# Kernel optimization log

Measured on AMD Instinct MI355X. Metric: run time of the kernel, lower is better.

## Reference

```python
import jax, jax.numpy as jnp
import numpy as np

VOCAB = 67
EMB = 32
BRANCH = 32
OUT = 96
L = 16
B = 131072


def setup_inputs() -> dict:
    key = jax.random.key(0)
    ks = jax.random.split(key, 10)
    x = jax.random.randint(ks[0], (B, L), 0, VOCAB, dtype=jnp.int64)
    embed = jax.random.normal(ks[1], (VOCAB, EMB), dtype=jnp.float32) * 0.1
    w2 = jax.random.normal(ks[2], (BRANCH, EMB, 2), dtype=jnp.float32) * 0.1
    b2 = jnp.zeros((BRANCH,), jnp.float32)
    w3 = jax.random.normal(ks[3], (BRANCH, EMB, 3), dtype=jnp.float32) * 0.1
    b3 = jnp.zeros((BRANCH,), jnp.float32)
    w4 = jax.random.normal(ks[4], (BRANCH, EMB, 4), dtype=jnp.float32) * 0.1
    b4 = jnp.zeros((BRANCH,), jnp.float32)
    pw = jax.random.normal(ks[5], (OUT, 3 * BRANCH), dtype=jnp.float32) * 0.02
    pb = jnp.zeros((OUT,), jnp.float32)
    return {"x": x, "embed": embed, "w2": w2, "b2": b2, "w3": w3,
            "b3": b3, "w4": w4, "b4": b4, "pw": pw, "pb": pb}


def _branch(emb_ncl, w, b):
    # emb_ncl: [B, EMB, L]; w: [BRANCH, EMB, k] -> conv valid, ReLU, max over time
    y = jax.lax.conv_general_dilated(
        emb_ncl, w, window_strides=(1,), padding='VALID',
        dimension_numbers=('NCH', 'OIH', 'NCH'))
    y = jax.nn.relu(y + b[None, :, None])
    return jnp.max(y, axis=2)  # [B, BRANCH]


def reference(x, embed, w2, b2, w3, b3, w4, b4, pw, pb):
    # padding_idx=0: row 0 of the table is zeros
    table = embed.at[0].set(0.0)
    emb = table[x]                      # [B, L, EMB]
    emb = jnp.transpose(emb, (0, 2, 1))  # [B, EMB, L]
    g2 = _branch(emb, w2, b2)
    g3 = _branch(emb, w3, b3)
    g4 = _branch(emb, w4, b4)
    feat = jnp.concatenate([g2, g3, g4], axis=1)  # [B, 96]
    # Linear + ReLU (dropout is identity at eval)
    return jax.nn.relu(feat @ pw.T + pb)
```

## Files before the change

### kernel.cpp

```cpp
#include <hip/hip_runtime.h>
#include <hip/hip_fp16.h>


#define VOCABSZ 67
#define EMBSZ   32
#define NCH     32
#define NFEAT   96
#define SEQL    16
#define BATCH   131072
#define NTAB    9
#define NENT    (NTAB * VOCABSZ)
#define TABU    (NENT * NCH / 2)
#define PWOFF   TABU
#define NFP     (NFEAT / 2)
#define NPW     (NFEAT * NFP)
#define ESTR    80
#define LTS     (VOCABSZ * ESTR)
#define LDSB    (NTAB * LTS)

typedef _Float16 v2h __attribute__((ext_vector_type(2)));
typedef _Float16 v8h __attribute__((ext_vector_type(8)));
typedef float    v4f __attribute__((ext_vector_type(4)));

__device__ __forceinline__ unsigned packh2(float a, float b) {
    v2h p; p[0] = (_Float16)a; p[1] = (_Float16)b;
    return __builtin_bit_cast(unsigned, p);
}

__global__ __launch_bounds__(256) void build_tables(
    const float* __restrict__ embed,
    const float* __restrict__ w2, const float* __restrict__ b2,
    const float* __restrict__ w3, const float* __restrict__ b3,
    const float* __restrict__ w4, const float* __restrict__ b4,
    const float* __restrict__ pw,
    unsigned* __restrict__ ws)
{
    int idx = blockIdx.x * 256 + threadIdx.x;
    if (idx < TABU) {
        int cp = idx & 15;
        int t  = idx >> 4;
        int j  = t / VOCABSZ;
        int v  = t - j * VOCABSZ;
        const float* w; const float* bias; int k, h;
        if (j < 2)      { w = w2; k = 2; h = j;     bias = (h == 0) ? b2 : nullptr; }
        else if (j < 5) { w = w3; k = 3; h = j - 2; bias = (h == 0) ? b3 : nullptr; }
        else            { w = w4; k = 4; h = j - 5; bias = (h == 0) ? b4 : nullptr; }
        int c0 = 2 * cp;
        float a0 = bias ? bias[c0]     : 0.0f;
        float a1 = bias ? bias[c0 + 1] : 0.0f;
        if (v != 0) {
            #pragma unroll
            for (int e = 0; e < EMBSZ; ++e) {
                float ev = embed[v * EMBSZ + e];
                a0 += ev * w[((c0    ) * EMBSZ + e) * k + h];
                a1 += ev * w[((c0 + 1) * EMBSZ + e) * k + h];
            }
        }
        ws[t * 16 + cp] = packh2(a0, a1);
    } else if (idx < TABU + NPW) {
        int i  = idx - TABU;
        int o  = i / NFP;
        int fp = i - o * NFP;
        ws[PWOFF + i] = packh2(pw[o * NFEAT + 2 * fp], pw[o * NFEAT + 2 * fp + 1]);
    }
}

template<int K, int N, int P0, int TB>
__device__ __forceinline__ void lconv(const char* __restrict__ base,
                                      const int (&ap)[16], v8h& m)
{
    v8h s[N];
    #pragma unroll
    for (int u = 0; u < N; ++u)
        s[u] = *reinterpret_cast<const v8h*>(base + TB + ap[P0 + u]);
    #pragma unroll
    for (int h = 1; h < K; ++h) {
        v8h t[N];
        #pragma unroll
        for (int u = 0; u < N; ++u)
            t[u] = *reinterpret_cast<const v8h*>(base + TB + h * LTS + ap[P0 + u + h]);
        #pragma unroll
        for (int u = 0; u < N; ++u) s[u] = s[u] + t[u];
    }
    #pragma unroll
    for (int u = 0; u < N; ++u) m = __builtin_elementwise_max(m, s[u]);
}

__global__ __launch_bounds__(512, 6) void fused_cnn(
    const int*      __restrict__ x,
    const unsigned* __restrict__ ws,
    const float*    __restrict__ pb,
    float*          __restrict__ out)
{
    extern __shared__ __align__(16) char ldsraw[];
    const int tid = threadIdx.x;
    {
        const float4* s4 = reinterpret_cast<const float4*>(ws);
        float4* d4 = reinterpret_cast<float4*>(ldsraw);
        #pragma unroll
        for (int i0 = 0; i0 < 2560; i0 += 512) {
            int i = i0 + tid;
            if (i < 2412) {
                int t = i >> 2, c = i & 3;
                d4[5 * t + c] = s4[i];
            }
        }
    }
    __syncthreads();

    const int lane = tid & 63;
    const int wv   = tid >> 6;
    const int ml   = lane & 15;
    const int c    = lane >> 4;
    const int co   = c << 4;
    const int rowb = blockIdx.x * 128 + wv * 16;
    const int row  = rowb + ml;
    const char* base = ldsraw;

    const int4* xp = reinterpret_cast<const int4*>(x + row * SEQL);
    int4 q0 = xp[0], q1 = xp[1], q2 = xp[2], q3 = xp[3];
    int ap[16];
    ap[ 0] = q0.x * ESTR + co; ap[ 1] = q0.y * ESTR + co;
    ap[ 2] = q0.z * ESTR + co; ap[ 3] = q0.w * ESTR + co;
    ap[ 4] = q1.x * ESTR + co; ap[ 5] = q1.y * ESTR + co;
    ap[ 6] = q1.z * ESTR + co; ap[ 7] = q1.w * ESTR + co;
    ap[ 8] = q2.x * ESTR + co; ap[ 9] = q2.y * ESTR + co;
    ap[10] = q2.z * ESTR + co; ap[11] = q2.w * ESTR + co;
    ap[12] = q3.x * ESTR + co; ap[13] = q3.y * ESTR + co;
    ap[14] = q3.z * ESTR + co; ap[15] = q3.w * ESTR + co;

    v8h m2 = {}, m3 = {}, m4 = {};

    lconv<2, 5,  0, 0 * LTS>(base, ap, m2);
    lconv<2, 5,  5, 0 * LTS>(base, ap, m2);
    lconv<2, 5, 10, 0 * LTS>(base, ap, m2);
    lconv<3, 5,  0, 2 * LTS>(base, ap, m3);
    lconv<3, 5,  5, 2 * LTS>(base, ap, m3);
    lconv<3, 4, 10, 2 * LTS>(base, ap, m3);
    lconv<4, 5,  0, 5 * LTS>(base, ap, m4);
    lconv<4, 4,  5, 5 * LTS>(base, ap, m4);
    lconv<4, 4,  9, 5 * LTS>(base, ap, m4);

    const unsigned* __restrict__ pwp = ws + PWOFF + ml * NFP + c * 4;
    #pragma unroll
    for (int u = 0; u < 6; ++u) {
        v4f acc = {0.f, 0.f, 0.f, 0.f};
        v8h b0 = *reinterpret_cast<const v8h*>(pwp + 768 * u);
        v8h b1 = *reinterpret_cast<const v8h*>(pwp + 768 * u + 16);
        v8h b2 = *reinterpret_cast<const v8h*>(pwp + 768 * u + 32);
        acc = __builtin_amdgcn_mfma_f32_16x16x32_f16(m2, b0, acc, 0, 0, 0);
        acc = __builtin_amdgcn_mfma_f32_16x16x32_f16(m3, b1, acc, 0, 0, 0);
        acc = __builtin_amdgcn_mfma_f32_16x16x32_f16(m4, b2, acc, 0, 0, 0);
        float pbl = pb[16 * u + ml];
        #pragma unroll
        for (int r = 0; r < 4; ++r)
            out[(size_t)(rowb + c * 4 + r) * NFEAT + 16 * u + ml] =
                fmaxf(acc[r] + pbl, 0.f);
    }
}

extern "C" void kernel_launch(void* const* d_in, const int* in_sizes, int n_in,
                              void* d_out, int out_size, void* d_ws, size_t ws_size,
                              hipStream_t stream)
{
    const int*   x     = (const int*)  d_in[0];
    const float* embed = (const float*)d_in[1];
    const float* w2    = (const float*)d_in[2];
    const float* b2    = (const float*)d_in[3];
    const float* w3    = (const float*)d_in[4];
    const float* b3    = (const float*)d_in[5];
    const float* w4    = (const float*)d_in[6];
    const float* b4    = (const float*)d_in[7];
    const float* pw    = (const float*)d_in[8];
    const float* pb    = (const float*)d_in[9];
    float* out = (float*)d_out;
    unsigned* ws = (unsigned*)d_ws;

    build_tables<<<(TABU + NPW + 255) / 256, 256, 0, stream>>>(
        embed, w2, b2, w3, b3, w4, b4, pw, ws);

    (void)hipFuncSetAttribute((const void*)fused_cnn,
                              hipFuncAttributeMaxDynamicSharedMemorySize,
                              LDSB);
    fused_cnn<<<BATCH / 128, 512, LDSB, stream>>>(x, ws, pb, out);
}
```

Measured before the change: 41.00 us.

## Precompute token-pair conv tables in global memory to halve gathers

Adds a build_pairs kernel that sums adjacent-tap per-token tables into 67x67 pair tables for the k=2, k=3 and k=4 branches. The main kernel then computes each window from one or two pair lookups in global memory (cache-resident), plus one LDS lookup for the third tap of k=3. LDS use drops to a single table, which may raise occupancy and shortens the LDS staging. The cost is an extra prep kernel, about 1.1 MB of pair tables read through L2 with random gathers, and a workspace-size check that falls back to the old LDS-only path if the workspace is too small.

Result: slower. 67.07 us (+63.6%).

```diff
diff --git a/kernel.cpp b/kernel.cpp
--- a/kernel.cpp
+++ b/kernel.cpp
@@ -14,9 +14,15 @@
 #define PWOFF   TABU
 #define NFP     (NFEAT / 2)
 #define NPW     (NFEAT * NFP)
+#define PAIRW   (TABU + NPW)
+#define NPAIR   (VOCABSZ * VOCABSZ)
+#define PRW     (NPAIR * 16)
+#define PRB     (NPAIR * 64)
+#define WSNEED  ((PAIRW + 4 * PRW) * 4)
 #define ESTR    80
 #define LTS     (VOCABSZ * ESTR)
-#define LDSB    (NTAB * LTS)
+#define LDSB9   LTS
+#define LDSB8   (NTAB * LTS)
 
 typedef _Float16 v2h __attribute__((ext_vector_type(2)));
 typedef _Float16 v8h __attribute__((ext_vector_type(8)));
@@ -65,6 +71,158 @@
     }
 }
 
+__global__ __launch_bounds__(256) void build_pairs(unsigned* __restrict__ ws)
+{
+    int idx = blockIdx.x * 256 + threadIdx.x;
+    if (idx >= 4 * PRW) return;
+    int g = idx / PRW;
+    int r = idx - g * PRW;
+    int e = r >> 4;
+    int w = r & 15;
+    int a = e / VOCABSZ;
+    int b = e - a * VOCABSZ;
+    int j0 = 2 * g + (g >> 1);
+    unsigned ua = ws[((j0    ) * VOCABSZ + a) * 16 + w];
+    unsigned ub = ws[((j0 + 1) * VOCABSZ + b) * 16 + w];
+    v2h s = __builtin_bit_cast(v2h, ua) + __builtin_bit_cast(v2h, ub);
+    ws[PAIRW + idx] = __builtin_bit_cast(unsigned, s);
+}
+
+template<int N, int P0>
+__device__ __forceinline__ void c2b(const char* __restrict__ g2,
+                                    const int (&pr)[15], v8h& m)
+{
+    v8h s[N];
+    #pragma unroll
+    for (int u = 0; u < N; ++u)
+        s[u] = *reinterpret_cast<const v8h*>(g2 + pr[P0 + u]);
+    #pragma unroll
+    for (int u = 0; u < N; ++u) m = __builtin_elementwise_max(m, s[u]);
+}
+
+template<int N, int P0>
+__device__ __forceinline__ void c3b(const char* __restrict__ g3,
+                                    const char* __restrict__ lb,
+                                    const int (&pr)[15], const int (&al)[14],
+                                    v8h& m)
+{
+    v8h s[N], t[N];
+    #pragma unroll
+    for (int u = 0; u < N; ++u)
+        s[u] = *reinterpret_cast<const v8h*>(g3 + pr[P0 + u]);
+    #pragma unroll
+    for (int u = 0; u < N; ++u)
+        t[u] = *reinterpret_cast<const v8h*>(lb + al[P0 + u]);
+    #pragma unroll
+    for (int u = 0; u < N; ++u)
+        m = __builtin_elementwise_max(m, s[u] + t[u]);
+}
+
+template<int N, int P0>
+__device__ __forceinline__ void c4b(const char* __restrict__ g4a,
+                                    const char* __restrict__ g4b,
+                                    const int (&pr)[15], v8h& m)
+{
+    v8h s[N], t[N];
+    #pragma unroll
+    for (int u = 0; u < N; ++u)
+        s[u] = *reinterpret_cast<const v8h*>(g4a + pr[P0 + u]);
+    #pragma unroll
+    for (int u = 0; u < N; ++u)
+        t[u] = *reinterpret_cast<const v8h*>(g4b + pr[P0 + u + 2]);
+    #pragma unroll
+    for (int u = 0; u < N; ++u)
+        m = __builtin_elementwise_max(m, s[u] + t[u]);
+}
+
+__global__ __launch_bounds__(512, 6) void fused_cnn(
+    const int*      __restrict__ x,
+    const unsigned* __restrict__ ws,
+    const float*    __restrict__ pb,
+    float*          __restrict__ out)
+{
+    extern __shared__ __align__(16) char ldsraw[];
+    const int tid = threadIdx.x;
+    {
+        const float4* s4 = reinterpret_cast<const float4*>(ws);
+        float4* d4 = reinterpret_cast<float4*>(ldsraw);
+        if (tid < 268) {
+            int v = tid >> 2, c = tid & 3;
+            d4[v * 5 + c] = s4[1072 + tid];
+        }
+    }
+    __syncthreads();
+
+    const int lane = tid & 63;
+    const int wv   = tid >> 6;
+    const int ml   = lane & 15;
+    const int c    = lane >> 4;
+    const int co   = c << 4;
+    const int rowb = blockIdx.x * 128 + wv * 16;
+    const int row  = rowb + ml;
+    const char* lb  = ldsraw;
+    const char* gp  = reinterpret_cast<const char*>(ws) + PAIRW * 4;
+    const char* g2  = gp;
+    const char* g3  = gp + PRB;
+    const char* g4a = gp + 2 * PRB;
+    const char* g4b = gp + 3 * PRB;
+
+    const int4* xp = reinterpret_cast<const int4*>(x + row * SEQL);
+    int4 q0 = xp[0], q1 = xp[1], q2 = xp[2], q3 = xp[3];
+    const int t0 = q0.x, t1 = q0.y, t2 = q0.z, t3 = q0.w;
+    const int t4 = q1.x, t5 = q1.y, t6 = q1.z, t7 = q1.w;
+    const int t8 = q2.x, t9 = q2.y, tA = q2.z, tB = q2.w;
+    const int tC = q3.x, tD = q3.y, tE = q3.z, tF = q3.w;
+
+    int pr[15];
+    pr[ 0] = (t0 * VOCABSZ + t1) * 64 + co; pr[ 1] = (t1 * VOCABSZ + t2) * 64 + co;
+    pr[ 2] = (t2 * VOCABSZ + t3) * 64 + co; pr[ 3] = (t3 * VOCABSZ + t4) * 64 + co;
+    pr[ 4] = (t4 * VOCABSZ + t5) * 64 + co; pr[ 5] = (t5 * VOCABSZ + t6) * 64 + co;
+    pr[ 6] = (t6 * VOCABSZ + t7) * 64 + co; pr[ 7] = (t7 * VOCABSZ + t8) * 64 + co;
+    pr[ 8] = (t8 * VOCABSZ + t9) * 64 + co; pr[ 9] = (t9 * VOCABSZ + tA) * 64 + co;
+    pr[10] = (tA * VOCABSZ + tB) * 64 + co; pr[11] = (tB * VOCABSZ + tC) * 64 + co;
+    pr[12] = (tC * VOCABSZ + tD) * 64 + co; pr[13] = (tD * VOCABSZ + tE) * 64 + co;
+    pr[14] = (tE * VOCABSZ + tF) * 64 + co;
+
+    int al[14];
+    al[ 0] = t2 * ESTR + co; al[ 1] = t3 * ESTR + co;
+    al[ 2] = t4 * ESTR + co; al[ 3] = t5 * ESTR + co;
+    al[ 4] = t6 * ESTR + co; al[ 5] = t7 * ESTR + co;
+    al[ 6] = t8 * ESTR + co; al[ 7] = t9 * ESTR + co;
+    al[ 8] = tA * ESTR + co; al[ 9] = tB * ESTR + co;
+    al[10] = tC * ESTR + co; al[11] = tD * ESTR + co;
+    al[12] = tE * ESTR + co; al[13] = tF * ESTR + co;
+
+    v8h m2 = {}, m3 = {}, m4 = {};
+
+    c2b<5,  0>(g2, pr, m2);
+    c4b<5,  0>(g4a, g4b, pr, m4);
+    c3b<5,  0>(g3, lb, pr, al, m3);
+    c2b<5,  5>(g2, pr, m2);
+    c4b<4,  5>(g4a, g4b, pr, m4);
+    c3b<5,  5>(g3, lb, pr, al, m3);
+    c2b<5, 10>(g2, pr, m2);
+    c4b<4,  9>(g4a, g4b, pr, m4);
+    c3b<4, 10>(g3, lb, pr, al, m3);
+
+    const unsigned* __restrict__ pwp = ws + PWOFF + ml * NFP + c * 4;
+    #pragma unroll
+    for (int u = 0; u < 6; ++u) {
+        v4f acc = {0.f, 0.f, 0.f, 0.f};
+        v8h b0 = *reinterpret_cast<const v8h*>(pwp + 768 * u);
+        v8h b1 = *reinterpret_cast<const v8h*>(pwp + 768 * u + 16);
+        v8h b2 = *reinterpret_cast<const v8h*>(pwp + 768 * u + 32);
+        acc = __builtin_amdgcn_mfma_f32_16x16x32_f16(m2, b0, acc, 0, 0, 0);
+        acc = __builtin_amdgcn_mfma_f32_16x16x32_f16(m3, b1, acc, 0, 0, 0);
+        acc = __builtin_amdgcn_mfma_f32_16x16x32_f16(m4, b2, acc, 0, 0, 0);
+        float pbl = pb[16 * u + ml];
+        #pragma unroll
+        for (int r = 0; r < 4; ++r)
+            out[(size_t)(rowb + c * 4 + r) * NFEAT + 16 * u + ml] =
+                fmaxf(acc[r] + pbl, 0.f);
+    }
+}
+
 template<int K, int N, int P0, int TB>
 __device__ __forceinline__ void lconv(const char* __restrict__ base,
                                       const int (&ap)[16], v8h& m)
@@ -86,7 +244,7 @@
     for (int u = 0; u < N; ++u) m = __builtin_elementwise_max(m, s[u]);
 }
 
-__global__ __launch_bounds__(512, 6) void fused_cnn(
+__global__ __launch_bounds__(512, 6) void fused_cnn_fb(
     const int*      __restrict__ x,
     const unsigned* __restrict__ ws,
     const float*    __restrict__ pb,
@@ -130,7 +288,6 @@
     ap[14] = q3.z * ESTR + co; ap[15] = q3.w * ESTR + co;
 
     v8h m2 = {}, m3 = {}, m4 = {};
-
     lconv<2, 5,  0, 0 * LTS>(base, ap, m2);
     lconv<2, 5,  5, 0 * LTS>(base, ap, m2);
     lconv<2, 5, 10, 0 * LTS>(base, ap, m2);
@@ -179,8 +336,10 @@
     build_tables<<<(TABU + NPW + 255) / 256, 256, 0, stream>>>(
         embed, w2, b2, w3, b3, w4, b4, pw, ws);
 
-    (void)hipFuncSetAttribute((const void*)fused_cnn,
-                              hipFuncAttributeMaxDynamicSharedMemorySize,
-                              LDSB);
-    fused_cnn<<<BATCH / 128, 512, LDSB, stream>>>(x, ws, pb, out);
-}
+    if (ws_size >= (size_t)WSNEED) {
+        build_pairs<<<(4 * PRW + 255) / 256, 256, 0, stream>>>(ws);
+        fused_cnn<<<BATCH / 128, 512, LDSB9, stream>>>(x, ws, pb, out);
+    } else {
+        fused_cnn_fb<<<BATCH / 128, 512, LDSB8, stream>>>(x, ws, pb, out);
+    }
+}
```

## Compute conv branches with MFMA on gathered embeddings instead of lookup tables

Applied to the files above, without the earlier changes.

Replaces the precomputed per-vocabulary conv lookup tables (summed with packed-half adds in LDS) with a direct MFMA convolution. The fp16 embedding table is staged in LDS, each lane gathers its sequence fragments, and per-tap weight fragments read from global memory are multiplied in with the bias folded into the accumulator. Pooled features pass through a per-wave LDS buffer to be rearranged for the projection MFMA. LDS use drops sharply, but matrix-core work rises, the occupancy hint is lowered to 3, and pooling now happens in fp32 before the fp16 store.

New measurement: 42.84 us. 4.5% more time.

```diff
diff --git a/kernel.cpp b/kernel.cpp
--- a/kernel.cpp
+++ b/kernel.cpp
@@ -8,15 +8,17 @@
 #define NFEAT   96
 #define SEQL    16
 #define BATCH   131072
-#define NTAB    9
-#define NENT    (NTAB * VOCABSZ)
-#define TABU    (NENT * NCH / 2)
-#define PWOFF   TABU
 #define NFP     (NFEAT / 2)
+#define EMBW    1072
+#define PWOFF_W EMBW
 #define NPW     (NFEAT * NFP)
-#define ESTR    80
-#define LTS     (VOCABSZ * ESTR)
-#define LDSB    (NTAB * LTS)
+#define BFOFF_W (PWOFF_W + NPW)
+#define NBF     18
+#define WSW     (BFOFF_W + NBF * 256)
+#define EMBLDS  (VOCABSZ * 128)
+#define FSTR    192
+#define FBUF    (16 * FSTR)
+#define LDSB    (EMBLDS + 8 * FBUF)
 
 typedef _Float16 v2h __attribute__((ext_vector_type(2)));
 typedef _Float16 v8h __attribute__((ext_vector_type(8)));
@@ -27,83 +29,91 @@
     return __builtin_bit_cast(unsigned, p);
 }
 
-__global__ __launch_bounds__(256) void build_tables(
+__global__ __launch_bounds__(256) void build_ws(
     const float* __restrict__ embed,
-    const float* __restrict__ w2, const float* __restrict__ b2,
-    const float* __restrict__ w3, const float* __restrict__ b3,
-    const float* __restrict__ w4, const float* __restrict__ b4,
-    const float* __restrict__ pw,
+    const float* __restrict__ w2, const float* __restrict__ w3,
+    const float* __restrict__ w4, const float* __restrict__ pw,
     unsigned* __restrict__ ws)
 {
     int idx = blockIdx.x * 256 + threadIdx.x;
-    if (idx < TABU) {
-        int cp = idx & 15;
-        int t  = idx >> 4;
-        int j  = t / VOCABSZ;
-        int v  = t - j * VOCABSZ;
-        const float* w; const float* bias; int k, h;
-        if (j < 2)      { w = w2; k = 2; h = j;     bias = (h == 0) ? b2 : nullptr; }
-        else if (j < 5) { w = w3; k = 3; h = j - 2; bias = (h == 0) ? b3 : nullptr; }
-        else            { w = w4; k = 4; h = j - 5; bias = (h == 0) ? b4 : nullptr; }
-        int c0 = 2 * cp;
-        float a0 = bias ? bias[c0]     : 0.0f;
-        float a1 = bias ? bias[c0 + 1] : 0.0f;
-        if (v != 0) {
-            #pragma unroll
-            for (int e = 0; e < EMBSZ; ++e) {
-                float ev = embed[v * EMBSZ + e];
-                a0 += ev * w[((c0    ) * EMBSZ + e) * k + h];
-                a1 += ev * w[((c0 + 1) * EMBSZ + e) * k + h];
-            }
-        }
-        ws[t * 16 + cp] = packh2(a0, a1);
-    } else if (idx < TABU + NPW) {
-        int i  = idx - TABU;
+    if (idx < EMBW) {
+        int v = idx >> 4, wd = idx & 15;
+        int e0 = 2 * wd;
+        ws[idx] = (v == 0) ? 0u
+                : packh2(embed[v * EMBSZ + e0], embed[v * EMBSZ + e0 + 1]);
+    } else if (idx < BFOFF_W) {
+        int i  = idx - PWOFF_W;
         int o  = i / NFP;
         int fp = i - o * NFP;
-        ws[PWOFF + i] = packh2(pw[o * NFEAT + 2 * fp], pw[o * NFEAT + 2 * fp + 1]);
+        ws[idx] = packh2(pw[o * NFEAT + 2 * fp], pw[o * NFEAT + 2 * fp + 1]);
+    } else if (idx < WSW) {
+        int i    = idx - BFOFF_W;
+        int fi   = i >> 8;
+        int l    = (i >> 2) & 63;
+        int wd   = i & 3;
+        const float* w; int k, t, nt;
+        if (fi < 4)       { w = w2; k = 2; t = fi >> 1;        nt = fi & 1; }
+        else if (fi < 10) { w = w3; k = 3; t = (fi - 4) >> 1;  nt = (fi - 4) & 1; }
+        else              { w = w4; k = 4; t = (fi - 10) >> 1; nt = (fi - 10) & 1; }
+        int ch = 16 * nt + (l & 15);
+        int e0 = 8 * (l >> 4) + 2 * wd;
+        ws[idx] = packh2(w[(ch * EMBSZ + e0    ) * k + t],
+                         w[(ch * EMBSZ + e0 + 1) * k + t]);
     }
 }
 
-template<int K, int N, int P0, int TB>
-__device__ __forceinline__ void lconv(const char* __restrict__ base,
-                                      const int (&ap)[16], v8h& m)
+template<int KT, int NP, int FI0, int CJ>
+__device__ __forceinline__ void convmm(const v8h (&frag)[16],
+                                       const char* __restrict__ bfr,
+                                       const float* __restrict__ bj,
+                                       char* fb, int lane)
 {
-    v8h s[N];
+    const int nl = lane & 15, g = lane >> 4;
     #pragma unroll
-    for (int u = 0; u < N; ++u)
-        s[u] = *reinterpret_cast<const v8h*>(base + TB + ap[P0 + u]);
-    #pragma unroll
-    for (int h = 1; h < K; ++h) {
-        v8h t[N];
+    for (int nt = 0; nt < 2; ++nt) {
+        float bv = bj[16 * nt + nl];
+        v8h B[KT];
         #pragma unroll
-        for (int u = 0; u < N; ++u)
-            t[u] = *reinterpret_cast<const v8h*>(base + TB + h * LTS + ap[P0 + u + h]);
+        for (int t = 0; t < KT; ++t)
+            B[t] = *reinterpret_cast<const v8h*>(
+                bfr + (FI0 + 2 * t + nt) * 1024 + lane * 16);
+        v4f mx = {0.f, 0.f, 0.f, 0.f};
         #pragma unroll
-        for (int u = 0; u < N; ++u) s[u] = s[u] + t[u];
+        for (int p = 0; p < NP; ++p) {
+            v4f acc = {bv, bv, bv, bv};
+            #pragma unroll
+            for (int t = 0; t < KT; ++t)
+                acc = __builtin_amdgcn_mfma_f32_16x16x32_f16(
+                    frag[p + t], B[t], acc, 0, 0, 0);
+            mx = __builtin_elementwise_max(mx, acc);
+        }
+        #pragma unroll
+        for (int r = 0; r < 4; ++r)
+            *reinterpret_cast<_Float16*>(
+                fb + (4 * g + r) * FSTR + (CJ * 32 + 16 * nt + nl) * 2) =
+                (_Float16)mx[r];
     }
-    #pragma unroll
-    for (int u = 0; u < N; ++u) m = __builtin_elementwise_max(m, s[u]);
 }
 
-__global__ __launch_bounds__(512, 6) void fused_cnn(
+__global__ __launch_bounds__(512, 3) void fused_cnn(
     const int*      __restrict__ x,
     const unsigned* __restrict__ ws,
+    const float*    __restrict__ b2,
+    const float*    __restrict__ b3,
+    const float*    __restrict__ b4,
     const float*    __restrict__ pb,
     float*          __restrict__ out)
 {
-    extern __shared__ __align__(16) char ldsraw[];
+    extern __shared__ __align__(16) char lds[];
     const int tid = threadIdx.x;
     {
         const float4* s4 = reinterpret_cast<const float4*>(ws);
-        float4* d4 = reinterpret_cast<float4*>(ldsraw);
-        #pragma unroll
-        for (int i0 = 0; i0 < 2560; i0 += 512) {
-            int i = i0 + tid;
-            if (i < 2412) {
-                int t = i >> 2, c = i & 3;
-                d4[5 * t + c] = s4[i];
-            }
+        float4* d4 = reinterpret_cast<float4*>(lds);
+        if (tid < 268) {
+            int v = tid >> 2, cw = tid & 3;
+            float4 e = s4[tid];
+            d4[v * 8 + cw]     = e;
+            d4[v * 8 + 4 + cw] = e;
         }
     }
     __syncthreads();
@@ -112,45 +122,43 @@
     const int wv   = tid >> 6;
     const int ml   = lane & 15;
     const int c    = lane >> 4;
-    const int co   = c << 4;
+    const int parc = (((lane >> 3) & 1) << 6) + (c << 4);
     const int rowb = blockIdx.x * 128 + wv * 16;
     const int row  = rowb + ml;
-    const char* base = ldsraw;
+    char* fb = lds + EMBLDS + wv * FBUF;
+    const char* bfr = reinterpret_cast<const char*>(ws + BFOFF_W);
 
     const int4* xp = reinterpret_cast<const int4*>(x + row * SEQL);
     int4 q0 = xp[0], q1 = xp[1], q2 = xp[2], q3 = xp[3];
-    int ap[16];
-    ap[ 0] = q0.x * ESTR + co; ap[ 1] = q0.y * ESTR + co;
-    ap[ 2] = q0.z * ESTR + co; ap[ 3] = q0.w * ESTR + co;
-    ap[ 4] = q1.x * ESTR + co; ap[ 5] = q1.y * ESTR + co;
-    ap[ 6] = q1.z * ESTR + co; ap[ 7] = q1.w * ESTR + co;
-    ap[ 8] = q2.x * ESTR + co; ap[ 9] = q2.y * ESTR + co;
-    ap[10] = q2.z * ESTR + co; ap[11] = q2.w * ESTR + co;
-    ap[12] = q3.x * ESTR + co; ap[13] = q3.y * ESTR + co;
-    ap[14] = q3.z * ESTR + co; ap[15] = q3.w * ESTR + co;
+    int tq[16];
+    tq[ 0] = q0.x; tq[ 1] = q0.y; tq[ 2] = q0.z; tq[ 3] = q0.w;
+    tq[ 4] = q1.x; tq[ 5] = q1.y; tq[ 6] = q1.z; tq[ 7] = q1.w;
+    tq[ 8] = q2.x; tq[ 9] = q2.y; tq[10] = q2.z; tq[11] = q2.w;
+    tq[12] = q3.x; tq[13] = q3.y; tq[14] = q3.z; tq[15] = q3.w;
 
-    v8h m2 = {}, m3 = {}, m4 = {};
+    v8h frag[16];
+    #pragma unroll
+    for (int q = 0; q < 16; ++q)
+        frag[q] = *reinterpret_cast<const v8h*>(lds + (tq[q] << 7) + parc);
 
-    lconv<2, 5,  0, 0 * LTS>(base, ap, m2);
-    lconv<2, 5,  5, 0 * LTS>(base, ap, m2);
-    lconv<2, 5, 10, 0 * LTS>(base, ap, m2);
-    lconv<3, 5,  0, 2 * LTS>(base, ap, m3);
-    lconv<3, 5,  5, 2 * LTS>(base, ap, m3);
-    lconv<3, 4, 10, 2 * LTS>(base, ap, m3);
-    lconv<4, 5,  0, 5 * LTS>(base, ap, m4);
-    lconv<4, 4,  5, 5 * LTS>(base, ap, m4);
-    lconv<4, 4,  9, 5 * LTS>(base, ap, m4);
+    convmm<2, 15,  0, 0>(frag, bfr, b2, fb, lane);
+    convmm<3, 14,  4, 1>(frag, bfr, b3, fb, lane);
+    convmm<4, 13, 10, 2>(frag, bfr, b4, fb, lane);
 
-    const unsigned* __restrict__ pwp = ws + PWOFF + ml * NFP + c * 4;
+    v8h m2 = *reinterpret_cast<const v8h*>(fb + ml * FSTR +       (c << 4));
+    v8h m3 = *reinterpret_cast<const v8h*>(fb + ml * FSTR +  64 + (c << 4));
+    v8h m4 = *reinterpret_cast<const v8h*>(fb + ml * FSTR + 128 + (c << 4));
+
+    const unsigned* __restrict__ pwp = ws + PWOFF_W + ml * NFP + c * 4;
     #pragma unroll
     for (int u = 0; u < 6; ++u) {
         v4f acc = {0.f, 0.f, 0.f, 0.f};
-        v8h b0 = *reinterpret_cast<const v8h*>(pwp + 768 * u);
-        v8h b1 = *reinterpret_cast<const v8h*>(pwp + 768 * u + 16);
-        v8h b2 = *reinterpret_cast<const v8h*>(pwp + 768 * u + 32);
-        acc = __builtin_amdgcn_mfma_f32_16x16x32_f16(m2, b0, acc, 0, 0, 0);
-        acc = __builtin_amdgcn_mfma_f32_16x16x32_f16(m3, b1, acc, 0, 0, 0);
-        acc = __builtin_amdgcn_mfma_f32_16x16x32_f16(m4, b2, acc, 0, 0, 0);
+        v8h w0 = *reinterpret_cast<const v8h*>(pwp + 768 * u);
+        v8h w1 = *reinterpret_cast<const v8h*>(pwp + 768 * u + 16);
+        v8h w2 = *reinterpret_cast<const v8h*>(pwp + 768 * u + 32);
+        acc = __builtin_amdgcn_mfma_f32_16x16x32_f16(m2, w0, acc, 0, 0, 0);
+        acc = __builtin_amdgcn_mfma_f32_16x16x32_f16(m3, w1, acc, 0, 0, 0);
+        acc = __builtin_amdgcn_mfma_f32_16x16x32_f16(m4, w2, acc, 0, 0, 0);
         float pbl = pb[16 * u + ml];
         #pragma unroll
         for (int r = 0; r < 4; ++r)
@@ -176,11 +184,7 @@
     float* out = (float*)d_out;
     unsigned* ws = (unsigned*)d_ws;
 
-    build_tables<<<(TABU + NPW + 255) / 256, 256, 0, stream>>>(
-        embed, w2, b2, w3, b3, w4, b4, pw, ws);
+    build_ws<<<(WSW + 255) / 256, 256, 0, stream>>>(embed, w2, w3, w4, pw, ws);
 
-    (void)hipFuncSetAttribute((const void*)fused_cnn,
-                              hipFuncAttributeMaxDynamicSharedMemorySize,
-                              LDSB);
-    fused_cnn<<<BATCH / 128, 512, LDSB, stream>>>(x, ws, pb, out);
+    fused_cnn<<<BATCH / 128, 512, LDSB, stream>>>(x, ws, b2, b3, b4, pb, out);
 }
```

## Precompute pairwise token tables for k=2/k=4 convs and use persistent blocks

Applied to the files above, without the earlier changes.

Adds a build_pairs3 kernel that precomputes summed fp16 conv contributions for every token pair (vocab²) for the k=2 branch and both halves of the k=4 branch, stored in global workspace. The main kernel then gathers pair entries from global/L2 instead of summing per-tap LDS entries, keeping only the k=3 branch in a duplicated LDS table. It also switches to 512 persistent blocks that each loop over two row tiles, and adds sched barriers to batch the loads. The cost is an extra kernel launch, a larger workspace and more global gathers, with the old kernel kept as a fallback when the workspace is too small.

After: 98.68 us. +140.7%, slower.

```diff
diff --git a/kernel.cpp b/kernel.cpp
--- a/kernel.cpp
+++ b/kernel.cpp
@@ -9,22 +9,32 @@
 #define SEQL    16
 #define BATCH   131072
 #define NTAB    9
-#define NENT    (NTAB * VOCABSZ)
-#define TABU    (NENT * NCH / 2)
-#define PWOFF   TABU
 #define NFP     (NFEAT / 2)
-#define NPW     (NFEAT * NFP)
+#define TABU    9648
+#define PWOFF   9648
+#define NPW     4608
+#define PAIRW   (TABU + NPW)
+#define NPAIR   (VOCABSZ * VOCABSZ)
+#define PRW     (NPAIR * 16)
+#define PRB     (NPAIR * 64)
+#define WSNEED  ((PAIRW + 3 * PRW) * 4)
+#define T3LDS   (201 * 128)
 #define ESTR    80
 #define LTS     (VOCABSZ * ESTR)
-#define LDSB    (NTAB * LTS)
+#define LDSB8   (NTAB * LTS)
 
 typedef _Float16 v2h __attribute__((ext_vector_type(2)));
 typedef _Float16 v8h __attribute__((ext_vector_type(8)));
 typedef float    v4f __attribute__((ext_vector_type(4)));
 
+#define SB() __builtin_amdgcn_sched_barrier(0)
+
 __device__ __forceinline__ unsigned packh2(float a, float b) {
     v2h p; p[0] = (_Float16)a; p[1] = (_Float16)b;
     return __builtin_bit_cast(unsigned, p);
+}
+__device__ __forceinline__ v8h vmax8(v8h a, v8h b) {
+    return __builtin_elementwise_max(a, b);
 }
 
 __global__ __launch_bounds__(256) void build_tables(
@@ -57,11 +67,142 @@
             }
         }
         ws[t * 16 + cp] = packh2(a0, a1);
-    } else if (idx < TABU + NPW) {
-        int i  = idx - TABU;
+    } else if (idx < PAIRW) {
+        int i  = idx - PWOFF;
         int o  = i / NFP;
         int fp = i - o * NFP;
-        ws[PWOFF + i] = packh2(pw[o * NFEAT + 2 * fp], pw[o * NFEAT + 2 * fp + 1]);
+        ws[idx] = packh2(pw[o * NFEAT + 2 * fp], pw[o * NFEAT + 2 * fp + 1]);
+    }
+}
+
+__global__ __launch_bounds__(256) void build_pairs3(unsigned* __restrict__ ws)
+{
+    int idx = blockIdx.x * 256 + threadIdx.x;
+    if (idx >= 3 * PRW) return;
+    int g = idx / PRW;
+    int r = idx - g * PRW;
+    int e = r >> 4;
+    int w = r & 15;
+    int a = e / VOCABSZ;
+    int b = e - a * VOCABSZ;
+    int j0 = (g == 0) ? 0 : (g == 1) ? 5 : 7;
+    unsigned ua = ws[((j0    ) * VOCABSZ + a) * 16 + w];
+    unsigned ub = ws[((j0 + 1) * VOCABSZ + b) * 16 + w];
+    v2h s = __builtin_bit_cast(v2h, ua) + __builtin_bit_cast(v2h, ub);
+    ws[PAIRW + idx] = __builtin_bit_cast(unsigned, s);
+}
+
+__global__ __launch_bounds__(512, 4) void fused_cnn(
+    const int*      __restrict__ x,
+    const unsigned* __restrict__ ws,
+    const float*    __restrict__ pb,
+    float*          __restrict__ out)
+{
+    __shared__ __align__(16) char lds[T3LDS];
+    const int tid = threadIdx.x;
+    {
+        const float4* s4 = reinterpret_cast<const float4*>(ws);
+        float4* d4 = reinterpret_cast<float4*>(lds);
+        for (int i = tid; i < 804; i += 512) {
+            int t = i >> 2, cc = i & 3;
+            float4 v = s4[536 + 4 * t + cc];
+            d4[t * 8 + cc]     = v;
+            d4[t * 8 + 4 + cc] = v;
+        }
+    }
+    __syncthreads();
+
+    const int lane = tid & 63;
+    const int wv   = tid >> 6;
+    const int ml   = lane & 15;
+    const int c    = lane >> 4;
+    const int co   = c << 4;
+    const int parc = (((lane >> 3) & 1) << 6) + co;
+    const char* g2  = reinterpret_cast<const char*>(ws + PAIRW);
+    const char* g4a = g2 + PRB;
+    const char* g4b = g2 + 2 * PRB;
+    const unsigned* __restrict__ pwp = ws + PWOFF + ml * NFP + c * 4;
+
+    #pragma unroll 1
+    for (int k = 0; k < 2; ++k) {
+        const int rowb = (blockIdx.x + k * 512) * 128 + wv * 16;
+        const int row  = rowb + ml;
+
+        const int4* xp = reinterpret_cast<const int4*>(x + row * SEQL);
+        int4 q0 = xp[0], q1 = xp[1], q2 = xp[2], q3 = xp[3];
+        int tq[16];
+        tq[ 0] = q0.x; tq[ 1] = q0.y; tq[ 2] = q0.z; tq[ 3] = q0.w;
+        tq[ 4] = q1.x; tq[ 5] = q1.y; tq[ 6] = q1.z; tq[ 7] = q1.w;
+        tq[ 8] = q2.x; tq[ 9] = q2.y; tq[10] = q2.z; tq[11] = q2.w;
+        tq[12] = q3.x; tq[13] = q3.y; tq[14] = q3.z; tq[15] = q3.w;
+
+        int pr[15];
+        #pragma unroll
+        for (int p = 0; p < 15; ++p)
+            pr[p] = tq[p] * 4288 + tq[p + 1] * 64 + co;
+
+        v8h A[15];
+        #pragma unroll
+        for (int p = 0; p < 15; ++p)
+            A[p] = *reinterpret_cast<const v8h*>(g2 + pr[p]);
+        SB();
+
+        v8h m3 = {};
+        #pragma unroll
+        for (int p = 0; p < 7; ++p) {
+            v8h s0 = *reinterpret_cast<const v8h*>(lds +        tq[p    ] * 128 + parc);
+            v8h s1 = *reinterpret_cast<const v8h*>(lds + 8576 + tq[p + 1] * 128 + parc);
+            v8h s2 = *reinterpret_cast<const v8h*>(lds + 17152 + tq[p + 2] * 128 + parc);
+            m3 = vmax8(m3, s0 + s1 + s2);
+        }
+        v8h m2 = {};
+        #pragma unroll
+        for (int p = 0; p < 15; ++p) m2 = vmax8(m2, A[p]);
+
+        v8h C[12];
+        #pragma unroll
+        for (int u = 0; u < 6; ++u) {
+            C[u]     = *reinterpret_cast<const v8h*>(g4a + pr[u]);
+            C[6 + u] = *reinterpret_cast<const v8h*>(g4b + pr[u + 2]);
+        }
+        SB();
+
+        #pragma unroll
+        for (int p = 7; p < 14; ++p) {
+            v8h s0 = *reinterpret_cast<const v8h*>(lds +        tq[p    ] * 128 + parc);
+            v8h s1 = *reinterpret_cast<const v8h*>(lds + 8576 + tq[p + 1] * 128 + parc);
+            v8h s2 = *reinterpret_cast<const v8h*>(lds + 17152 + tq[p + 2] * 128 + parc);
+            m3 = vmax8(m3, s0 + s1 + s2);
+        }
+        v8h m4 = {};
+        #pragma unroll
+        for (int u = 0; u < 6; ++u) m4 = vmax8(m4, C[u] + C[6 + u]);
+
+        v8h D[14];
+        #pragma unroll
+        for (int u = 0; u < 7; ++u) {
+            D[u]     = *reinterpret_cast<const v8h*>(g4a + pr[6 + u]);
+            D[7 + u] = *reinterpret_cast<const v8h*>(g4b + pr[8 + u]);
+        }
+        SB();
+        #pragma unroll
+        for (int u = 0; u < 7; ++u) m4 = vmax8(m4, D[u] + D[7 + u]);
+
+        #pragma unroll
+        for (int u = 0; u < 6; ++u) {
+            v4f acc = {0.f, 0.f, 0.f, 0.f};
+            v8h w0 = *reinterpret_cast<const v8h*>(pwp + 768 * u);
+            v8h w1 = *reinterpret_cast<const v8h*>(pwp + 768 * u + 16);
+            v8h w2 = *reinterpret_cast<const v8h*>(pwp + 768 * u + 32);
+            acc = __builtin_amdgcn_mfma_f32_16x16x32_f16(m2, w0, acc, 0, 0, 0);
+            acc = __builtin_amdgcn_mfma_f32_16x16x32_f16(m3, w1, acc, 0, 0, 0);
+            acc = __builtin_amdgcn_mfma_f32_16x16x32_f16(m4, w2, acc, 0, 0, 0);
+            float pbl = pb[16 * u + ml];
+            #pragma unroll
+            for (int r = 0; r < 4; ++r)
+                out[(size_t)(rowb + c * 4 + r) * NFEAT + 16 * u + ml] =
+                    fmaxf(acc[r] + pbl, 0.f);
+        }
     }
 }
 
@@ -86,7 +227,7 @@
     for (int u = 0; u < N; ++u) m = __builtin_elementwise_max(m, s[u]);
 }
 
-__global__ __launch_bounds__(512, 6) void fused_cnn(
+__global__ __launch_bounds__(512, 6) void fused_cnn_fb(
     const int*      __restrict__ x,
     const unsigned* __restrict__ ws,
     const float*    __restrict__ pb,
@@ -101,8 +242,8 @@
         for (int i0 = 0; i0 < 2560; i0 += 512) {
             int i = i0 + tid;
             if (i < 2412) {
-                int t = i >> 2, c = i & 3;
-                d4[5 * t + c] = s4[i];
+                int t = i >> 2, cc = i & 3;
+                d4[5 * t + cc] = s4[i];
             }
         }
     }
@@ -130,7 +271,6 @@
     ap[14] = q3.z * ESTR + co; ap[15] = q3.w * ESTR + co;
 
     v8h m2 = {}, m3 = {}, m4 = {};
-
     lconv<2, 5,  0, 0 * LTS>(base, ap, m2);
     lconv<2, 5,  5, 0 * LTS>(base, ap, m2);
     lconv<2, 5, 10, 0 * LTS>(base, ap, m2);
@@ -145,12 +285,12 @@
     #pragma unroll
     for (int u = 0; u < 6; ++u) {
         v4f acc = {0.f, 0.f, 0.f, 0.f};
-        v8h b0 = *reinterpret_cast<const v8h*>(pwp + 768 * u);
-        v8h b1 = *reinterpret_cast<const v8h*>(pwp + 768 * u + 16);
-        v8h b2 = *reinterpret_cast<const v8h*>(pwp + 768 * u + 32);
-        acc = __builtin_amdgcn_mfma_f32_16x16x32_f16(m2, b0, acc, 0, 0, 0);
-        acc = __builtin_amdgcn_mfma_f32_16x16x32_f16(m3, b1, acc, 0, 0, 0);
-        acc = __builtin_amdgcn_mfma_f32_16x16x32_f16(m4, b2, acc, 0, 0, 0);
+        v8h w0 = *reinterpret_cast<const v8h*>(pwp + 768 * u);
+        v8h w1 = *reinterpret_cast<const v8h*>(pwp + 768 * u + 16);
+        v8h w2 = *reinterpret_cast<const v8h*>(pwp + 768 * u + 32);
+        acc = __builtin_amdgcn_mfma_f32_16x16x32_f16(m2, w0, acc, 0, 0, 0);
+        acc = __builtin_amdgcn_mfma_f32_16x16x32_f16(m3, w1, acc, 0, 0, 0);
+        acc = __builtin_amdgcn_mfma_f32_16x16x32_f16(m4, w2, acc, 0, 0, 0);
         float pbl = pb[16 * u + ml];
         #pragma unroll
         for (int r = 0; r < 4; ++r)
@@ -176,11 +316,16 @@
     float* out = (float*)d_out;
     unsigned* ws = (unsigned*)d_ws;
 
-    build_tables<<<(TABU + NPW + 255) / 256, 256, 0, stream>>>(
+    build_tables<<<(PAIRW + 255) / 256, 256, 0, stream>>>(
         embed, w2, b2, w3, b3, w4, b4, pw, ws);
 
-    (void)hipFuncSetAttribute((const void*)fused_cnn,
-                              hipFuncAttributeMaxDynamicSharedMemorySize,
-                              LDSB);
-    fused_cnn<<<BATCH / 128, 512, LDSB, stream>>>(x, ws, pb, out);
-}
+    if (ws_size >= (size_t)WSNEED) {
+        build_pairs3<<<(3 * PRW + 255) / 256, 256, 0, stream>>>(ws);
+        fused_cnn<<<512, 512, 0, stream>>>(x, ws, pb, out);
+    } else {
+        (void)hipFuncSetAttribute((const void*)fused_cnn_fb,
+                                  hipFuncAttributeMaxDynamicSharedMemorySize,
+                                  LDSB8);
+        fused_cnn_fb<<<BATCH / 128, 512, LDSB8, stream>>>(x, ws, pb, out);
+    }
+}
```
